# Performance work log

Hardware: AMD Instinct MI355X
Metric: run time of the kernel (lower is better)

Reference implementation:

```python
import jax, jax.numpy as jnp
import numpy as np

EPS = 1e-5  # torch LayerNorm default eps

def _mish(x):
    return x * jnp.tanh(jax.nn.softplus(x))

def _ln(x, g, b):
    mu = jnp.mean(x, axis=-1, keepdims=True)
    var = jnp.mean(jnp.square(x - mu), axis=-1, keepdims=True)
    return (x - mu) * jax.lax.rsqrt(var + EPS) * g + b

def setup_inputs() -> dict:
    key = jax.random.key(0)
    ks = jax.random.split(key, 10)
    B, D, O1, O2, O3 = 65536, 784, 512, 264, 128
    def lin(k, fan_in, shape):
        bound = 1.0 / np.sqrt(fan_in)
        return jax.random.uniform(k, shape, jnp.float32, -bound, bound)
    return {
        "x":  jax.random.uniform(ks[0], (B, D), jnp.float32),
        "W1": lin(ks[1], D,  (O1, D)),   # enFC1, bias=False
        "g1": jnp.ones((O1,), jnp.float32), "b1": jnp.zeros((O1,), jnp.float32),
        "W2": lin(ks[2], O1, (O2, O1)),  # enFC2, bias=False
        "g2": jnp.ones((O2,), jnp.float32), "b2": jnp.zeros((O2,), jnp.float32),
        "W3": lin(ks[3], O2, (O3, O2)),  # enFC3 with bias
        "b3": lin(ks[4], O2, (O3,)),
        "gh": jnp.ones((O3,), jnp.float32), "bh": jnp.zeros((O3,), jnp.float32),
        "D1": lin(ks[5], O3, (O2, O3)),  # deFC1, bias=False
        "g3": jnp.ones((O2,), jnp.float32), "b3n": jnp.zeros((O2,), jnp.float32),
        "D2": lin(ks[6], O2, (O1, O2)),  # deFC2, bias=False
        "g4": jnp.ones((O1,), jnp.float32), "b4": jnp.zeros((O1,), jnp.float32),
        "D3": lin(ks[7], O1, (D, O1)),   # deFC3 with bias
        "bo": lin(ks[8], O1, (D,)),
    }

def reference(x, W1, g1, b1, W2, g2, b2, W3, b3, gh, bh,
              D1, g3, b3n, D2, g4, b4, D3, bo):
    h = _mish(_ln(x @ W1.T, g1, b1))
    h = _mish(_ln(h @ W2.T, g2, b2))
    x_latent = _mish(_ln(h @ W3.T + b3, gh, bh))
    h = _mish(_ln(x_latent @ D1.T, g3, b3n))
    h = _mish(_ln(h @ D2.T, g4, b4))
    out = jax.nn.sigmoid(h @ D3.T + bo)
    return out, jnp.sum(jnp.abs(x_latent))
```

## Files before the change

### kernel.cpp

```cpp
#include <hip/hip_runtime.h>


typedef short bf16x8 __attribute__((ext_vector_type(8)));
typedef float f32x4  __attribute__((ext_vector_type(4)));

#define B_ROWS 65536
#define EPS_LN 1e-5f

static __device__ __forceinline__ unsigned short f2bf(float f) {
    union { float f; unsigned u; } v; v.f = f;
    unsigned r = v.u + 0x7FFFu + ((v.u >> 16) & 1u);
    return (unsigned short)(r >> 16);
}

static __device__ __forceinline__ float mish_f(float x) {
    if (x > 15.f) return x;
    float u = __expf(x);
    float p = __fmaf_rn(u, u, 2.f * u);
    return x * (p / (p + 2.f));
}

static __device__ __forceinline__ void glds16(const void* g, void* l) {
    typedef __attribute__((address_space(3))) unsigned lds_u32;
    typedef __attribute__((address_space(1))) const unsigned glb_u32;
    lds_u32* lp = (lds_u32*)l;
    unsigned lofs = __builtin_amdgcn_readfirstlane((unsigned)(unsigned long long)lp);
    lp = (lds_u32*)(unsigned long long)lofs;
    __builtin_amdgcn_global_load_lds((glb_u32*)g, lp, 16, 0, 0);
}

struct CvtArgs {
    const float* src[6];
    unsigned short* dst[6];
    int O[6], K[6], KP[6];
    int base[7];
};

__global__ void wpad_kernel(CvtArgs a) {
    int b = blockIdx.x;
    int seg = 0;
    while (b >= a.base[seg + 1]) ++seg;
    int r = b - a.base[seg];
    int O = a.O[seg], K = a.K[seg], KP = a.KP[seg];
    const float* s = a.src[seg];
    unsigned short* d = a.dst[seg];
    for (int c = threadIdx.x; c < KP; c += 256) {
        unsigned short v = 0;
        if (r < O && c < K) v = f2bf(s[(size_t)r * K + c]);
        d[(size_t)r * KP + c] = v;
    }
}

template<int KP, int ASTR, int KREAL, int OP, int OREAL, int OSTRIDE, int NKT,
         int NW, int WR, bool SRCF32, bool HASBIAS, bool ABS, bool LN>
__global__ __launch_bounds__(NW * 64, 4)
void layer5(const void* __restrict__ Asrc,
            const unsigned short* __restrict__ Wp,
            const float* __restrict__ gam,
            const float* __restrict__ bet,
            const float* __restrict__ bias,
            void* __restrict__ Aout,
            float* __restrict__ partials)
{
    constexpr int WC    = NW / WR;
    constexpr int NT    = OP / (WC * 16);
    constexpr int AR    = 4 / WR;
    constexpr int WROWS = 16 * AR;
    constexpr int NCH_W = OP / 16;
    constexpr int NCH   = NCH_W + (SRCF32 ? 0 : 4);
    constexpr int MAXC  = (NCH + NW - 1) / NW;
    constexpr int ABY   = 4096;
    constexpr int WBY   = OP * 64;

    __shared__ __align__(16) char smem[2 * ABY + 2 * WBY];

    const int tid  = threadIdx.x;
    const int wave = tid >> 6, lane = tid & 63;
    const int wrI = wave / WC, wcI = wave % WC;
    const int lg = lane >> 4, lc = lane & 15;
    const int row0  = blockIdx.x * 64;
    const int cbase = blockIdx.y * OP;

    const char* gp[MAXC];
#pragma unroll
    for (int i = 0; i < MAXC; ++i) {
        int c = wave + NW * i;
        gp[i] = nullptr;
        if (c < NCH_W) {
            int row = c * 16 + (lane >> 2);
            int sg = (lane & 3) ^ ((row >> 1) & 3);
            gp[i] = (const char*)Wp + ((size_t)(cbase + row) * KP + sg * 8) * 2;
        } else if (c < NCH) {
            int row = (c - NCH_W) * 16 + (lane >> 2);
            int sg = (lane & 3) ^ ((row >> 1) & 3);
            gp[i] = (const char*)Asrc + ((size_t)(row0 + row) * ASTR + sg * 8) * 2;
        }
    }
    auto stage = [&](int t, int b) {
#pragma unroll
        for (int i = 0; i < MAXC; ++i) {
            int c = wave + NW * i;
            if (c < NCH) {
                int off = (c < NCH_W) ? (2 * ABY + b * WBY + c * 1024)
                                      : (b * ABY + (c - NCH_W) * 1024);
                glds16(gp[i] + (size_t)t * 64, smem + off);
            }
        }
    };

    const int ar = tid >> 2, as = tid & 3;
    const float* axp = (const float*)Asrc + (size_t)(row0 + ar) * ASTR + as * 8;
    const int aswz = ar * 64 + ((as ^ ((ar >> 1) & 3)) << 4);
    float4 rA0 = make_float4(0,0,0,0), rA1 = make_float4(0,0,0,0);

    auto loadA1 = [&](int t) {
        int c0 = t * 32 + as * 8;
        rA0 = (c0     < KREAL) ? *(const float4*)(axp + t * 32)     : make_float4(0,0,0,0);
        rA1 = (c0 + 4 < KREAL) ? *(const float4*)(axp + t * 32 + 4) : make_float4(0,0,0,0);
    };
    auto pubA = [&](int b) {
        union { unsigned short us[8]; uint4 v; } u;
        u.us[0] = f2bf(rA0.x); u.us[1] = f2bf(rA0.y);
        u.us[2] = f2bf(rA0.z); u.us[3] = f2bf(rA0.w);
        u.us[4] = f2bf(rA1.x); u.us[5] = f2bf(rA1.y);
        u.us[6] = f2bf(rA1.z); u.us[7] = f2bf(rA1.w);
        *(uint4*)(smem + b * ABY + aswz) = u.v;
    };

    stage(0, 0);
    if constexpr (SRCF32) {
        if (tid < 256) { loadA1(0); pubA(0); if (NKT > 1) loadA1(1); }
    }
    __syncthreads();

    f32x4 acc[AR][NT];
#pragma unroll
    for (int a = 0; a < AR; ++a)
#pragma unroll
        for (int c = 0; c < NT; ++c) acc[a][c] = (f32x4){0.f, 0.f, 0.f, 0.f};

    const int fswz = ((lg ^ ((lc >> 1) & 3)) << 4);

    for (int t = 0; t < NKT; ++t) {
        const int bsel = t & 1;
        if (t + 1 < NKT) stage(t + 1, bsel ^ 1);

        const char* Ab = smem + bsel * ABY + (wrI * WROWS + lc) * 64 + fswz;
        const char* Bb = smem + 2 * ABY + bsel * WBY + (wcI * NT * 16 + lc) * 64 + fswz;
        bf16x8 afr[AR], bfr[NT];
#pragma unroll
        for (int a = 0; a < AR; ++a) afr[a] = *(const bf16x8*)(Ab + a * 1024);
#pragma unroll
        for (int c = 0; c < NT; ++c) bfr[c] = *(const bf16x8*)(Bb + c * 1024);

        if constexpr (SRCF32) {
            if (tid < 256) {
                if (t + 1 < NKT) pubA(bsel ^ 1);
                if (t + 2 < NKT) loadA1(t + 2);
            }
        }
#pragma unroll
        for (int c = 0; c < NT; ++c)
#pragma unroll
            for (int a = 0; a < AR; ++a)
                acc[a][c] = __builtin_amdgcn_mfma_f32_16x16x32_bf16(afr[a], bfr[c], acc[a][c], 0, 0, 0);
        __syncthreads();
    }

    if constexpr (LN) {
        if constexpr (HASBIAS) {
#pragma unroll
            for (int c = 0; c < NT; ++c) {
                int col = wcI * NT * 16 + c * 16 + lc;
                float bv = (col < OREAL) ? bias[col] : 0.f;
#pragma unroll
                for (int a = 0; a < AR; ++a)
#pragma unroll
                    for (int r = 0; r < 4; ++r) acc[a][c][r] += bv;
            }
        }
        float ps1[AR][4], ps2[AR][4];
#pragma unroll
        for (int a = 0; a < AR; ++a)
#pragma unroll
            for (int r = 0; r < 4; ++r) { ps1[a][r] = 0.f; ps2[a][r] = 0.f; }
#pragma unroll
        for (int a = 0; a < AR; ++a)
#pragma unroll
            for (int c = 0; c < NT; ++c)
#pragma unroll
                for (int r = 0; r < 4; ++r) {
                    float v = acc[a][c][r];
                    ps1[a][r] += v;
                    ps2[a][r] = __fmaf_rn(v, v, ps2[a][r]);
                }
#pragma unroll
        for (int m = 1; m < 16; m <<= 1)
#pragma unroll
            for (int a = 0; a < AR; ++a)
#pragma unroll
                for (int r = 0; r < 4; ++r) {
                    ps1[a][r] += __shfl_xor(ps1[a][r], m);
                    ps2[a][r] += __shfl_xor(ps2[a][r], m);
                }

        float* lnP   = (float*)smem;
        float* lnMR  = (float*)smem + 1024;
        float* wsumP = (float*)smem + 1152;

        if (lc == 0) {
#pragma unroll
            for (int a = 0; a < AR; ++a)
#pragma unroll
                for (int r = 0; r < 4; ++r) {
                    int row = a * 16 + lg * 4 + r;
                    lnP[row * 8 + wcI]       = ps1[a][r];
                    lnP[512 + row * 8 + wcI] = ps2[a][r];
                }
        }
        __syncthreads();
        if (tid < 64) {
            float s1 = 0.f, s2 = 0.f;
#pragma unroll
            for (int w = 0; w < WC; ++w) { s1 += lnP[tid * 8 + w]; s2 += lnP[512 + tid * 8 + w]; }
            float mu = s1 * (1.f / OREAL);
            float var = fmaxf(s2 * (1.f / OREAL) - mu * mu, 0.f);
            lnMR[tid]      = mu;
            lnMR[64 + tid] = rsqrtf(var + EPS_LN);
        }
        __syncthreads();

        float gcol[NT], bcol[NT];
#pragma unroll
        for (int c = 0; c < NT; ++c) {
            int col = wcI * NT * 16 + c * 16 + lc;
            gcol[c] = (col < OREAL) ? gam[col] : 0.f;
            bcol[c] = (col < OREAL) ? bet[col] : 0.f;
        }

        float asum = 0.f;
        unsigned short* outp = (unsigned short*)Aout;
#pragma unroll
        for (int a = 0; a < AR; ++a)
#pragma unroll
            for (int r = 0; r < 4; ++r) {
                int rl = a * 16 + lg * 4 + r;
                float mu = lnMR[rl], rs = lnMR[64 + rl];
                size_t rowoff = (size_t)(row0 + rl) * OSTRIDE;
#pragma unroll
                for (int c = 0; c < NT; ++c) {
                    int col = wcI * NT * 16 + c * 16 + lc;
                    if (col < OSTRIDE) {
                        unsigned short outv = 0;
                        if (col < OREAL) {
                            float v = (acc[a][c][r] - mu) * rs * gcol[c] + bcol[c];
                            float mz = mish_f(v);
                            if (ABS) asum += fabsf(mz);
                            outv = f2bf(mz);
                        }
                        outp[rowoff + col] = outv;
                    }
                }
            }

        if constexpr (ABS) {
#pragma unroll
            for (int m = 1; m < 64; m <<= 1) asum += __shfl_xor(asum, m);
            if (lane == 0) wsumP[wave] = asum;
            __syncthreads();
            if (tid == 0) {
                float s = 0.f;
                for (int w = 0; w < NW; ++w) s += wsumP[w];
                partials[blockIdx.x] = s;
            }
        }
    } else {
        float* outp = (float*)Aout;
#pragma unroll
        for (int c = 0; c < NT; ++c) {
            int col = cbase + wcI * NT * 16 + c * 16 + lc;
            bool ok = col < OREAL;
            float bv = ok ? bias[col] : 0.f;
#pragma unroll
            for (int a = 0; a < AR; ++a)
#pragma unroll
                for (int r = 0; r < 4; ++r) {
                    if (ok) {
                        int rl = wrI * WROWS + a * 16 + lg * 4 + r;
                        float v = acc[a][c][r] + bv;
                        outp[(size_t)(row0 + rl) * OSTRIDE + col] = 1.f / (1.f + __expf(-v));
                    }
                }
        }
    }
}

__global__ void reduce_abs(const float* __restrict__ partials, float* __restrict__ out) {
    __shared__ float sm[256];
    float s = 0.f;
    for (int i = threadIdx.x; i < 1024; i += 256) s += partials[i];
    sm[threadIdx.x] = s;
    __syncthreads();
    for (int step = 128; step > 0; step >>= 1) {
        if (threadIdx.x < step) sm[threadIdx.x] += sm[threadIdx.x + step];
        __syncthreads();
    }
    if (threadIdx.x == 0) out[0] = sm[0];
}

extern "C" void kernel_launch(void* const* d_in, const int* in_sizes, int n_in,
                              void* d_out, int out_size, void* d_ws, size_t ws_size,
                              hipStream_t stream)
{
    const float* x   = (const float*)d_in[0];
    const float* W1  = (const float*)d_in[1];
    const float* g1  = (const float*)d_in[2];
    const float* b1  = (const float*)d_in[3];
    const float* W2  = (const float*)d_in[4];
    const float* g2  = (const float*)d_in[5];
    const float* b2  = (const float*)d_in[6];
    const float* W3  = (const float*)d_in[7];
    const float* b3  = (const float*)d_in[8];
    const float* gh  = (const float*)d_in[9];
    const float* bh  = (const float*)d_in[10];
    const float* D1  = (const float*)d_in[11];
    const float* g3  = (const float*)d_in[12];
    const float* b3n = (const float*)d_in[13];
    const float* D2  = (const float*)d_in[14];
    const float* g4  = (const float*)d_in[15];
    const float* b4  = (const float*)d_in[16];
    const float* D3  = (const float*)d_in[17];
    const float* bo  = (const float*)d_in[18];

    char* ws = (char*)d_ws;
    size_t off = 0;
    auto alloc = [&](size_t bytes) -> char* {
        char* p = ws + off;
        off += (bytes + 255) & ~(size_t)255;
        return p;
    };
    unsigned short* W1p = (unsigned short*)alloc((size_t)512 * 800 * 2);
    unsigned short* W2p = (unsigned short*)alloc((size_t)384 * 512 * 2);
    unsigned short* W3p = (unsigned short*)alloc((size_t)128 * 288 * 2);
    unsigned short* D1p = (unsigned short*)alloc((size_t)384 * 128 * 2);
    unsigned short* D2p = (unsigned short*)alloc((size_t)512 * 288 * 2);
    unsigned short* D3p = (unsigned short*)alloc((size_t)896 * 512 * 2);
    unsigned short* actP = (unsigned short*)alloc((size_t)B_ROWS * 512 * 2);
    unsigned short* actQ = (unsigned short*)alloc((size_t)B_ROWS * 288 * 2);
    unsigned short* actL = (unsigned short*)alloc((size_t)B_ROWS * 128 * 2);
    float* partials = (float*)alloc(1024 * 4);

    CvtArgs ca;
    ca.src[0] = W1; ca.dst[0] = W1p; ca.O[0] = 512; ca.K[0] = 784; ca.KP[0] = 800;
    ca.src[1] = W2; ca.dst[1] = W2p; ca.O[1] = 264; ca.K[1] = 512; ca.KP[1] = 512;
    ca.src[2] = W3; ca.dst[2] = W3p; ca.O[2] = 128; ca.K[2] = 264; ca.KP[2] = 288;
    ca.src[3] = D1; ca.dst[3] = D1p; ca.O[3] = 264; ca.K[3] = 128; ca.KP[3] = 128;
    ca.src[4] = D2; ca.dst[4] = D2p; ca.O[4] = 512; ca.K[4] = 264; ca.KP[4] = 288;
    ca.src[5] = D3; ca.dst[5] = D3p; ca.O[5] = 784; ca.K[5] = 512; ca.KP[5] = 512;
    ca.base[0] = 0;    ca.base[1] = 512;  ca.base[2] = 896;
    ca.base[3] = 1024; ca.base[4] = 1408; ca.base[5] = 1920; ca.base[6] = 2816;
    wpad_kernel<<<2816, 256, 0, stream>>>(ca);

    const int NB = B_ROWS / 64;

    layer5<800, 784, 784, 512, 512, 512, 25, 8, 1, true,  false, false, true>
        <<<NB, 512, 0, stream>>>(x, W1p, g1, b1, nullptr, actP, nullptr);
    layer5<512, 512, 512, 384, 264, 288, 16, 8, 1, false, false, false, true>
        <<<NB, 512, 0, stream>>>(actP, W2p, g2, b2, nullptr, actQ, nullptr);
    layer5<288, 288, 288, 128, 128, 128, 9,  4, 1, false, true,  true,  true>
        <<<NB, 256, 0, stream>>>(actQ, W3p, gh, bh, b3, actL, partials);
    layer5<128, 128, 128, 384, 264, 288, 4,  8, 1, false, false, false, true>
        <<<NB, 512, 0, stream>>>(actL, D1p, g3, b3n, nullptr, actQ, nullptr);
    layer5<288, 288, 288, 512, 512, 512, 9,  8, 1, false, false, false, true>
        <<<NB, 512, 0, stream>>>(actQ, D2p, g4, b4, nullptr, actP, nullptr);
    dim3 g6(NB, 4);
    layer5<512, 512, 512, 224, 784, 784, 16, 4, 2, false, true,  false, false>
        <<<g6, 256, 0, stream>>>(actP, D3p, nullptr, nullptr, bo, d_out, nullptr);

    reduce_abs<<<1, 256, 0, stream>>>(partials, (float*)d_out + (size_t)B_ROWS * 784);
}
```

Measured before the change: 485.6 us.

## Use 16-wave blocks for all layers and pre-convert input to bf16

Adds a separate kernel that converts x to bf16 once, so the first layer can stage A through direct global-to-LDS loads instead of converting in-kernel from fp32. Every layer kernel now runs with 1024 threads (16 waves), which rearranges the wave-to-tile mapping and the LayerNorm partial reductions. The final layer is split into two launches over column ranges instead of a 4-wide grid. This trades an extra full pass over x (read fp32, write bf16) and larger blocks with higher register pressure for more in-flight waves and simpler staging.

```diff
diff --git a/kernel.cpp b/kernel.cpp
--- a/kernel.cpp
+++ b/kernel.cpp
@@ -27,6 +27,17 @@
     unsigned lofs = __builtin_amdgcn_readfirstlane((unsigned)(unsigned long long)lp);
     lp = (lds_u32*)(unsigned long long)lofs;
     __builtin_amdgcn_global_load_lds((glb_u32*)g, lp, 16, 0, 0);
+}
+
+__global__ __launch_bounds__(256)
+void cvtx_kernel(const float* __restrict__ x, unsigned short* __restrict__ xb) {
+    size_t i = ((size_t)blockIdx.x * 256 + threadIdx.x) * 8;
+    float4 a = *(const float4*)(x + i);
+    float4 b = *(const float4*)(x + i + 4);
+    union { unsigned short us[8]; uint4 v; } u;
+    u.us[0] = f2bf(a.x); u.us[1] = f2bf(a.y); u.us[2] = f2bf(a.z); u.us[3] = f2bf(a.w);
+    u.us[4] = f2bf(b.x); u.us[5] = f2bf(b.y); u.us[6] = f2bf(b.z); u.us[7] = f2bf(b.w);
+    *(uint4*)(xb + i) = u.v;
 }
 
 struct CvtArgs {
@@ -51,86 +62,60 @@
     }
 }
 
-template<int KP, int ASTR, int KREAL, int OP, int OREAL, int OSTRIDE, int NKT,
-         int NW, int WR, bool SRCF32, bool HASBIAS, bool ABS, bool LN>
-__global__ __launch_bounds__(NW * 64, 4)
-void layer5(const void* __restrict__ Asrc,
+template<int KP, int ASTR, int OP, int OREAL, int OSTRIDE, int NKT,
+         int WR, bool HASBIAS, bool ABS, bool LN>
+__global__ __launch_bounds__(1024, 8)
+void layer6(const unsigned short* __restrict__ Asrc,
             const unsigned short* __restrict__ Wp,
             const float* __restrict__ gam,
             const float* __restrict__ bet,
             const float* __restrict__ bias,
             void* __restrict__ Aout,
-            float* __restrict__ partials)
+            float* __restrict__ partials,
+            int cbase)
 {
-    constexpr int WC    = NW / WR;
+    constexpr int WC    = 16 / WR;
     constexpr int NT    = OP / (WC * 16);
     constexpr int AR    = 4 / WR;
     constexpr int WROWS = 16 * AR;
     constexpr int NCH_W = OP / 16;
-    constexpr int NCH   = NCH_W + (SRCF32 ? 0 : 4);
-    constexpr int MAXC  = (NCH + NW - 1) / NW;
+    constexpr int NCH   = NCH_W + 4;
+    constexpr int MAXC  = (NCH + 15) / 16;
     constexpr int ABY   = 4096;
     constexpr int WBY   = OP * 64;
 
     __shared__ __align__(16) char smem[2 * ABY + 2 * WBY];
 
     const int tid  = threadIdx.x;
-    const int wave = tid >> 6, lane = tid & 63;
-    const int wrI = wave / WC, wcI = wave % WC;
+    const int lane = tid & 63;
+    const int wu   = __builtin_amdgcn_readfirstlane(tid >> 6);
+    const int wrI = wu / WC, wcI = wu % WC;
     const int lg = lane >> 4, lc = lane & 15;
-    const int row0  = blockIdx.x * 64;
-    const int cbase = blockIdx.y * OP;
-
-    const char* gp[MAXC];
-#pragma unroll
-    for (int i = 0; i < MAXC; ++i) {
-        int c = wave + NW * i;
-        gp[i] = nullptr;
-        if (c < NCH_W) {
-            int row = c * 16 + (lane >> 2);
-            int sg = (lane & 3) ^ ((row >> 1) & 3);
-            gp[i] = (const char*)Wp + ((size_t)(cbase + row) * KP + sg * 8) * 2;
-        } else if (c < NCH) {
-            int row = (c - NCH_W) * 16 + (lane >> 2);
-            int sg = (lane & 3) ^ ((row >> 1) & 3);
-            gp[i] = (const char*)Asrc + ((size_t)(row0 + row) * ASTR + sg * 8) * 2;
-        }
-    }
+    const int row0 = blockIdx.x * 64;
+
+    const size_t vofW = (size_t)(((lane >> 2) * KP   + (((lane & 3) ^ ((lane >> 3) & 3)) << 3)) * 2);
+    const size_t vofA = (size_t)(((lane >> 2) * ASTR + (((lane & 3) ^ ((lane >> 3) & 3)) << 3)) * 2);
+
     auto stage = [&](int t, int b) {
 #pragma unroll
         for (int i = 0; i < MAXC; ++i) {
-            int c = wave + NW * i;
+            int c = wu + 16 * i;
             if (c < NCH) {
-                int off = (c < NCH_W) ? (2 * ABY + b * WBY + c * 1024)
-                                      : (b * ABY + (c - NCH_W) * 1024);
-                glds16(gp[i] + (size_t)t * 64, smem + off);
+                if (c < NCH_W) {
+                    const char* g = (const char*)Wp +
+                        ((size_t)(cbase + c * 16) * KP) * 2 + (size_t)t * 64 + vofW;
+                    glds16(g, smem + (2 * ABY + b * WBY + c * 1024));
+                } else {
+                    int ca = c - NCH_W;
+                    const char* g = (const char*)Asrc +
+                        ((size_t)(row0 + ca * 16) * ASTR) * 2 + (size_t)t * 64 + vofA;
+                    glds16(g, smem + (b * ABY + ca * 1024));
+                }
             }
         }
     };
 
-    const int ar = tid >> 2, as = tid & 3;
-    const float* axp = (const float*)Asrc + (size_t)(row0 + ar) * ASTR + as * 8;
-    const int aswz = ar * 64 + ((as ^ ((ar >> 1) & 3)) << 4);
-    float4 rA0 = make_float4(0,0,0,0), rA1 = make_float4(0,0,0,0);
-
-    auto loadA1 = [&](int t) {
-        int c0 = t * 32 + as * 8;
-        rA0 = (c0     < KREAL) ? *(const float4*)(axp + t * 32)     : make_float4(0,0,0,0);
-        rA1 = (c0 + 4 < KREAL) ? *(const float4*)(axp + t * 32 + 4) : make_float4(0,0,0,0);
-    };
-    auto pubA = [&](int b) {
-        union { unsigned short us[8]; uint4 v; } u;
-        u.us[0] = f2bf(rA0.x); u.us[1] = f2bf(rA0.y);
-        u.us[2] = f2bf(rA0.z); u.us[3] = f2bf(rA0.w);
-        u.us[4] = f2bf(rA1.x); u.us[5] = f2bf(rA1.y);
-        u.us[6] = f2bf(rA1.z); u.us[7] = f2bf(rA1.w);
-        *(uint4*)(smem + b * ABY + aswz) = u.v;
-    };
-
     stage(0, 0);
-    if constexpr (SRCF32) {
-        if (tid < 256) { loadA1(0); pubA(0); if (NKT > 1) loadA1(1); }
-    }
     __syncthreads();
 
     f32x4 acc[AR][NT];
@@ -153,12 +138,6 @@
 #pragma unroll
         for (int c = 0; c < NT; ++c) bfr[c] = *(const bf16x8*)(Bb + c * 1024);
 
-        if constexpr (SRCF32) {
-            if (tid < 256) {
-                if (t + 1 < NKT) pubA(bsel ^ 1);
-                if (t + 2 < NKT) loadA1(t + 2);
-            }
-        }
 #pragma unroll
         for (int c = 0; c < NT; ++c)
 #pragma unroll
@@ -205,24 +184,27 @@
                 }
 
         float* lnP   = (float*)smem;
-        float* lnMR  = (float*)smem + 1024;
-        float* wsumP = (float*)smem + 1152;
+        float* lnMR  = (float*)(smem + 8192);
+        float* wsumP = (float*)(smem + 8192 + 512);
 
         if (lc == 0) {
 #pragma unroll
             for (int a = 0; a < AR; ++a)
 #pragma unroll
                 for (int r = 0; r < 4; ++r) {
-                    int row = a * 16 + lg * 4 + r;
-                    lnP[row * 8 + wcI]       = ps1[a][r];
-                    lnP[512 + row * 8 + wcI] = ps2[a][r];
+                    int rl = wrI * WROWS + a * 16 + lg * 4 + r;
+                    lnP[rl * WC + wcI]           = ps1[a][r];
+                    lnP[64 * WC + rl * WC + wcI] = ps2[a][r];
                 }
         }
         __syncthreads();
         if (tid < 64) {
             float s1 = 0.f, s2 = 0.f;
 #pragma unroll
-            for (int w = 0; w < WC; ++w) { s1 += lnP[tid * 8 + w]; s2 += lnP[512 + tid * 8 + w]; }
+            for (int w = 0; w < WC; ++w) {
+                s1 += lnP[tid * WC + w];
+                s2 += lnP[64 * WC + tid * WC + w];
+            }
             float mu = s1 * (1.f / OREAL);
             float var = fmaxf(s2 * (1.f / OREAL) - mu * mu, 0.f);
             lnMR[tid]      = mu;
@@ -244,7 +226,7 @@
         for (int a = 0; a < AR; ++a)
 #pragma unroll
             for (int r = 0; r < 4; ++r) {
-                int rl = a * 16 + lg * 4 + r;
+                int rl = wrI * WROWS + a * 16 + lg * 4 + r;
                 float mu = lnMR[rl], rs = lnMR[64 + rl];
                 size_t rowoff = (size_t)(row0 + rl) * OSTRIDE;
 #pragma unroll
@@ -266,11 +248,11 @@
         if constexpr (ABS) {
 #pragma unroll
             for (int m = 1; m < 64; m <<= 1) asum += __shfl_xor(asum, m);
-            if (lane == 0) wsumP[wave] = asum;
+            if (lane == 0) wsumP[tid >> 6] = asum;
             __syncthreads();
             if (tid == 0) {
                 float s = 0.f;
-                for (int w = 0; w < NW; ++w) s += wsumP[w];
+                for (int w = 0; w < 16; ++w) s += wsumP[w];
                 partials[blockIdx.x] = s;
             }
         }
@@ -345,10 +327,13 @@
     unsigned short* D1p = (unsigned short*)alloc((size_t)384 * 128 * 2);
     unsigned short* D2p = (unsigned short*)alloc((size_t)512 * 288 * 2);
     unsigned short* D3p = (unsigned short*)alloc((size_t)896 * 512 * 2);
-    unsigned short* actP = (unsigned short*)alloc((size_t)B_ROWS * 512 * 2);
-    unsigned short* actQ = (unsigned short*)alloc((size_t)B_ROWS * 288 * 2);
-    unsigned short* actL = (unsigned short*)alloc((size_t)B_ROWS * 128 * 2);
+    unsigned short* xbf = (unsigned short*)alloc((size_t)B_ROWS * 784 * 2 + 256);
+    unsigned short* actP = (unsigned short*)alloc((size_t)B_ROWS * 512 * 2 + 256);
+    unsigned short* actQ = (unsigned short*)alloc((size_t)B_ROWS * 288 * 2 + 256);
+    unsigned short* actL = (unsigned short*)alloc((size_t)B_ROWS * 128 * 2 + 256);
     float* partials = (float*)alloc(1024 * 4);
+
+    cvtx_kernel<<<25088, 256, 0, stream>>>(x, xbf);
 
     CvtArgs ca;
     ca.src[0] = W1; ca.dst[0] = W1p; ca.O[0] = 512; ca.K[0] = 784; ca.KP[0] = 800;
@@ -363,19 +348,20 @@
 
     const int NB = B_ROWS / 64;
 
-    layer5<800, 784, 784, 512, 512, 512, 25, 8, 1, true,  false, false, true>
-        <<<NB, 512, 0, stream>>>(x, W1p, g1, b1, nullptr, actP, nullptr);
-    layer5<512, 512, 512, 384, 264, 288, 16, 8, 1, false, false, false, true>
-        <<<NB, 512, 0, stream>>>(actP, W2p, g2, b2, nullptr, actQ, nullptr);
-    layer5<288, 288, 288, 128, 128, 128, 9,  4, 1, false, true,  true,  true>
-        <<<NB, 256, 0, stream>>>(actQ, W3p, gh, bh, b3, actL, partials);
-    layer5<128, 128, 128, 384, 264, 288, 4,  8, 1, false, false, false, true>
-        <<<NB, 512, 0, stream>>>(actL, D1p, g3, b3n, nullptr, actQ, nullptr);
-    layer5<288, 288, 288, 512, 512, 512, 9,  8, 1, false, false, false, true>
-        <<<NB, 512, 0, stream>>>(actQ, D2p, g4, b4, nullptr, actP, nullptr);
-    dim3 g6(NB, 4);
-    layer5<512, 512, 512, 224, 784, 784, 16, 4, 2, false, true,  false, false>
-        <<<g6, 256, 0, stream>>>(actP, D3p, nullptr, nullptr, bo, d_out, nullptr);
+    layer6<800, 784, 512, 512, 512, 25, 1, false, false, true>
+        <<<NB, 1024, 0, stream>>>(xbf, W1p, g1, b1, nullptr, actP, nullptr, 0);
+    layer6<512, 512, 384, 264, 288, 16, 2, false, false, true>
+        <<<NB, 1024, 0, stream>>>(actP, W2p, g2, b2, nullptr, actQ, nullptr, 0);
+    layer6<288, 288, 128, 128, 128, 9, 2, true, true, true>
+        <<<NB, 1024, 0, stream>>>(actQ, W3p, gh, bh, b3, actL, partials, 0);
+    layer6<128, 128, 384, 264, 288, 4, 2, false, false, true>
+        <<<NB, 1024, 0, stream>>>(actL, D1p, g3, b3n, nullptr, actQ, nullptr, 0);
+    layer6<288, 288, 512, 512, 512, 9, 1, false, false, true>
+        <<<NB, 1024, 0, stream>>>(actQ, D2p, g4, b4, nullptr, actP, nullptr, 0);
+    layer6<512, 512, 512, 784, 784, 16, 1, true, false, false>
+        <<<NB, 1024, 0, stream>>>(actP, D3p, nullptr, nullptr, bo, d_out, nullptr, 0);
+    layer6<512, 512, 384, 784, 784, 16, 2, true, false, false>
+        <<<NB, 1024, 0, stream>>>(actP, D3p, nullptr, nullptr, bo, d_out, nullptr, 512);
 
     reduce_abs<<<1, 256, 0, stream>>>(partials, (float*)d_out + (size_t)B_ROWS * 784);
 }
```

Result: slower. 636.5 us (+31.1%).

## Fuse all six MLP layers into one persistent-per-tile megakernel with LDS activations

Applied to the files above, without the earlier changes.

Replaces six separate layer launches with a single 1024-thread kernel per 64-row tile. The tile's intermediate activations stay in LDS (about 148 KB) and are never written to or reread from global memory. This targets the HBM traffic for the bf16 intermediates and the per-launch overhead. The cost is one block per CU with a large LDS footprint, lower occupancy, and weights restaged from global/L2 for every tile, so latency hiding depends on the in-block double buffering.

```diff
diff --git a/kernel.cpp b/kernel.cpp
--- a/kernel.cpp
+++ b/kernel.cpp
@@ -51,72 +51,87 @@
     }
 }
 
-template<int KP, int ASTR, int KREAL, int OP, int OREAL, int OSTRIDE, int NKT,
-         int NW, int WR, bool SRCF32, bool HASBIAS, bool ABS, bool LN>
-__global__ __launch_bounds__(NW * 64, 4)
-void layer5(const void* __restrict__ Asrc,
-            const unsigned short* __restrict__ Wp,
-            const float* __restrict__ gam,
-            const float* __restrict__ bet,
-            const float* __restrict__ bias,
-            void* __restrict__ Aout,
-            float* __restrict__ partials)
-{
-    constexpr int WC    = NW / WR;
-    constexpr int NT    = OP / (WC * 16);
-    constexpr int AR    = 4 / WR;
-    constexpr int WROWS = 16 * AR;
-    constexpr int NCH_W = OP / 16;
-    constexpr int NCH   = NCH_W + (SRCF32 ? 0 : 4);
-    constexpr int MAXC  = (NCH + NW - 1) / NW;
-    constexpr int ABY   = 4096;
-    constexpr int WBY   = OP * 64;
-
-    __shared__ __align__(16) char smem[2 * ABY + 2 * WBY];
-
-    const int tid  = threadIdx.x;
-    const int wave = tid >> 6, lane = tid & 63;
-    const int wrI = wave / WC, wcI = wave % WC;
-    const int lg = lane >> 4, lc = lane & 15;
-    const int row0  = blockIdx.x * 64;
-    const int cbase = blockIdx.y * OP;
-
-    const char* gp[MAXC];
-#pragma unroll
-    for (int i = 0; i < MAXC; ++i) {
-        int c = wave + NW * i;
-        gp[i] = nullptr;
-        if (c < NCH_W) {
-            int row = c * 16 + (lane >> 2);
-            int sg = (lane & 3) ^ ((row >> 1) & 3);
-            gp[i] = (const char*)Wp + ((size_t)(cbase + row) * KP + sg * 8) * 2;
-        } else if (c < NCH) {
-            int row = (c - NCH_W) * 16 + (lane >> 2);
-            int sg = (lane & 3) ^ ((row >> 1) & 3);
-            gp[i] = (const char*)Asrc + ((size_t)(row0 + row) * ASTR + sg * 8) * 2;
-        }
-    }
+template<int NKT, int OP, int KP, int WSTB, bool WDB, int ABASE, int ASTRLDS>
+__device__ __forceinline__ void gemm_h(char* smem,
+    const unsigned short* __restrict__ Wp, int cbase,
+    int lane, int wu, int wrI, int wcI, int lg, int lc, int fswz,
+    f32x4 (&acc)[2][OP / 128])
+{
+    constexpr int NT = OP / 128, NCHW = OP / 16, MAXC = (NCHW + 15) / 16;
+    constexpr int WBY = OP * 64;
+    const size_t vofW = ((size_t)(lane >> 2) * KP +
+                         (size_t)((((lane & 3) ^ ((lane >> 3) & 3))) << 3)) * 2;
     auto stage = [&](int t, int b) {
 #pragma unroll
         for (int i = 0; i < MAXC; ++i) {
-            int c = wave + NW * i;
-            if (c < NCH) {
-                int off = (c < NCH_W) ? (2 * ABY + b * WBY + c * 1024)
-                                      : (b * ABY + (c - NCH_W) * 1024);
-                glds16(gp[i] + (size_t)t * 64, smem + off);
+            int c = wu + 16 * i;
+            if (c < NCHW) {
+                const char* g = (const char*)Wp +
+                    ((size_t)(cbase + c * 16) * KP) * 2 + (size_t)t * 64 + vofW;
+                glds16(g, smem + WSTB + (WDB ? b * WBY : 0) + c * 1024);
             }
         }
     };
-
+    if constexpr (WDB) stage(0, 0);
+    __syncthreads();
+    for (int t = 0; t < NKT; ++t) {
+        int bsel = 0;
+        if constexpr (WDB) {
+            bsel = t & 1;
+            if (t + 1 < NKT) stage(t + 1, bsel ^ 1);
+        } else {
+            stage(t, 0);
+            __syncthreads();
+        }
+        bf16x8 afr[2], bfr[NT];
+#pragma unroll
+        for (int a = 0; a < 2; ++a) {
+            int arow = wrI * 32 + a * 16 + lc;
+            afr[a] = *(const bf16x8*)(smem + ABASE + arow * ASTRLDS + t * 64 + fswz);
+        }
+#pragma unroll
+        for (int c = 0; c < NT; ++c) {
+            int wrow = wcI * (NT * 16) + c * 16 + lc;
+            bfr[c] = *(const bf16x8*)(smem + WSTB + (WDB ? bsel * WBY : 0) + wrow * 64 + fswz);
+        }
+#pragma unroll
+        for (int c = 0; c < NT; ++c)
+#pragma unroll
+            for (int a = 0; a < 2; ++a)
+                acc[a][c] = __builtin_amdgcn_mfma_f32_16x16x32_bf16(afr[a], bfr[c], acc[a][c], 0, 0, 0);
+        __syncthreads();
+    }
+}
+
+template<int NKT, int OP, int KP, int WSTB, int ABASE>
+__device__ __forceinline__ void gemm_f32(char* smem,
+    const unsigned short* __restrict__ Wp, const float* __restrict__ x, int row0,
+    int tid, int lane, int wu, int wrI, int wcI, int lg, int lc, int fswz,
+    f32x4 (&acc)[2][OP / 128])
+{
+    constexpr int NT = OP / 128, NCHW = OP / 16, MAXC = (NCHW + 15) / 16;
+    constexpr int WBY = OP * 64;
+    const size_t vofW = ((size_t)(lane >> 2) * KP +
+                         (size_t)((((lane & 3) ^ ((lane >> 3) & 3))) << 3)) * 2;
+    auto stage = [&](int t, int b) {
+#pragma unroll
+        for (int i = 0; i < MAXC; ++i) {
+            int c = wu + 16 * i;
+            if (c < NCHW) {
+                const char* g = (const char*)Wp +
+                    ((size_t)c * 16 * KP) * 2 + (size_t)t * 64 + vofW;
+                glds16(g, smem + WSTB + b * WBY + c * 1024);
+            }
+        }
+    };
     const int ar = tid >> 2, as = tid & 3;
-    const float* axp = (const float*)Asrc + (size_t)(row0 + ar) * ASTR + as * 8;
+    const float* axp = x + (size_t)(row0 + ar) * 784 + as * 8;
     const int aswz = ar * 64 + ((as ^ ((ar >> 1) & 3)) << 4);
-    float4 rA0 = make_float4(0,0,0,0), rA1 = make_float4(0,0,0,0);
-
+    float4 rA0 = make_float4(0, 0, 0, 0), rA1 = make_float4(0, 0, 0, 0);
     auto loadA1 = [&](int t) {
         int c0 = t * 32 + as * 8;
-        rA0 = (c0     < KREAL) ? *(const float4*)(axp + t * 32)     : make_float4(0,0,0,0);
-        rA1 = (c0 + 4 < KREAL) ? *(const float4*)(axp + t * 32 + 4) : make_float4(0,0,0,0);
+        rA0 = (c0     < 784) ? *(const float4*)(axp + t * 32)     : make_float4(0, 0, 0, 0);
+        rA1 = (c0 + 4 < 784) ? *(const float4*)(axp + t * 32 + 4) : make_float4(0, 0, 0, 0);
     };
     auto pubA = [&](int b) {
         union { unsigned short us[8]; uint4 v; } u;
@@ -124,174 +139,269 @@
         u.us[2] = f2bf(rA0.z); u.us[3] = f2bf(rA0.w);
         u.us[4] = f2bf(rA1.x); u.us[5] = f2bf(rA1.y);
         u.us[6] = f2bf(rA1.z); u.us[7] = f2bf(rA1.w);
-        *(uint4*)(smem + b * ABY + aswz) = u.v;
+        *(uint4*)(smem + ABASE + b * 4096 + aswz) = u.v;
     };
-
     stage(0, 0);
-    if constexpr (SRCF32) {
-        if (tid < 256) { loadA1(0); pubA(0); if (NKT > 1) loadA1(1); }
-    }
-    __syncthreads();
-
-    f32x4 acc[AR][NT];
-#pragma unroll
-    for (int a = 0; a < AR; ++a)
-#pragma unroll
-        for (int c = 0; c < NT; ++c) acc[a][c] = (f32x4){0.f, 0.f, 0.f, 0.f};
-
-    const int fswz = ((lg ^ ((lc >> 1) & 3)) << 4);
-
+    if (tid < 256) { loadA1(0); pubA(0); if (NKT > 1) loadA1(1); }
+    __syncthreads();
     for (int t = 0; t < NKT; ++t) {
         const int bsel = t & 1;
         if (t + 1 < NKT) stage(t + 1, bsel ^ 1);
-
-        const char* Ab = smem + bsel * ABY + (wrI * WROWS + lc) * 64 + fswz;
-        const char* Bb = smem + 2 * ABY + bsel * WBY + (wcI * NT * 16 + lc) * 64 + fswz;
-        bf16x8 afr[AR], bfr[NT];
-#pragma unroll
-        for (int a = 0; a < AR; ++a) afr[a] = *(const bf16x8*)(Ab + a * 1024);
-#pragma unroll
-        for (int c = 0; c < NT; ++c) bfr[c] = *(const bf16x8*)(Bb + c * 1024);
-
-        if constexpr (SRCF32) {
-            if (tid < 256) {
-                if (t + 1 < NKT) pubA(bsel ^ 1);
-                if (t + 2 < NKT) loadA1(t + 2);
-            }
+        bf16x8 afr[2], bfr[NT];
+#pragma unroll
+        for (int a = 0; a < 2; ++a) {
+            int arow = wrI * 32 + a * 16 + lc;
+            afr[a] = *(const bf16x8*)(smem + ABASE + bsel * 4096 + arow * 64 + fswz);
+        }
+#pragma unroll
+        for (int c = 0; c < NT; ++c) {
+            int wrow = wcI * (NT * 16) + c * 16 + lc;
+            bfr[c] = *(const bf16x8*)(smem + WSTB + bsel * WBY + wrow * 64 + fswz);
+        }
+        if (tid < 256) {
+            if (t + 1 < NKT) pubA(bsel ^ 1);
+            if (t + 2 < NKT) loadA1(t + 2);
         }
 #pragma unroll
         for (int c = 0; c < NT; ++c)
 #pragma unroll
-            for (int a = 0; a < AR; ++a)
+            for (int a = 0; a < 2; ++a)
                 acc[a][c] = __builtin_amdgcn_mfma_f32_16x16x32_bf16(afr[a], bfr[c], acc[a][c], 0, 0, 0);
         __syncthreads();
     }
-
-    if constexpr (LN) {
-        if constexpr (HASBIAS) {
+}
+
+template<int OP, int OREAL, int OSTR, int HBASE, int HSTR, int SCR, bool HB, bool ABS>
+__device__ __forceinline__ void ln_epi(char* smem, f32x4 (&acc)[2][OP / 128],
+    const float* __restrict__ gam, const float* __restrict__ bet,
+    const float* __restrict__ bias, float* __restrict__ partials,
+    int tid, int lane, int wu, int wrI, int wcI, int lg, int lc, int bidx)
+{
+    constexpr int NT = OP / 128;
+    if constexpr (HB) {
+#pragma unroll
+        for (int c = 0; c < NT; ++c) {
+            int col = wcI * (NT * 16) + c * 16 + lc;
+            float bv = (col < OREAL) ? bias[col] : 0.f;
+#pragma unroll
+            for (int a = 0; a < 2; ++a)
+#pragma unroll
+                for (int r = 0; r < 4; ++r) acc[a][c][r] += bv;
+        }
+    }
+    float ps1[2][4], ps2[2][4];
+#pragma unroll
+    for (int a = 0; a < 2; ++a)
+#pragma unroll
+        for (int r = 0; r < 4; ++r) { ps1[a][r] = 0.f; ps2[a][r] = 0.f; }
+#pragma unroll
+    for (int a = 0; a < 2; ++a)
+#pragma unroll
+        for (int c = 0; c < NT; ++c)
+#pragma unroll
+            for (int r = 0; r < 4; ++r) {
+                float v = acc[a][c][r];
+                ps1[a][r] += v;
+                ps2[a][r] = __fmaf_rn(v, v, ps2[a][r]);
+            }
+#pragma unroll
+    for (int m = 1; m < 16; m <<= 1)
+#pragma unroll
+        for (int a = 0; a < 2; ++a)
+#pragma unroll
+            for (int r = 0; r < 4; ++r) {
+                ps1[a][r] += __shfl_xor(ps1[a][r], m);
+                ps2[a][r] += __shfl_xor(ps2[a][r], m);
+            }
+    float* lnP  = (float*)(smem + SCR);
+    float* lnMR = (float*)(smem + SCR + 4096);
+    float* wsum = (float*)(smem + SCR + 4608);
+    if (lc == 0) {
+#pragma unroll
+        for (int a = 0; a < 2; ++a)
+#pragma unroll
+            for (int r = 0; r < 4; ++r) {
+                int row = wrI * 32 + a * 16 + lg * 4 + r;
+                lnP[row * 8 + wcI]       = ps1[a][r];
+                lnP[512 + row * 8 + wcI] = ps2[a][r];
+            }
+    }
+    __syncthreads();
+    if (tid < 64) {
+        float s1 = 0.f, s2 = 0.f;
+#pragma unroll
+        for (int w = 0; w < 8; ++w) { s1 += lnP[tid * 8 + w]; s2 += lnP[512 + tid * 8 + w]; }
+        float mu = s1 * (1.f / OREAL);
+        float var = fmaxf(s2 * (1.f / OREAL) - mu * mu, 0.f);
+        lnMR[tid]      = mu;
+        lnMR[64 + tid] = rsqrtf(var + EPS_LN);
+    }
+    __syncthreads();
+    float gcol[NT], bcol[NT];
+#pragma unroll
+    for (int c = 0; c < NT; ++c) {
+        int col = wcI * (NT * 16) + c * 16 + lc;
+        gcol[c] = (col < OREAL) ? gam[col] : 0.f;
+        bcol[c] = (col < OREAL) ? bet[col] : 0.f;
+    }
+    float asum = 0.f;
+#pragma unroll
+    for (int a = 0; a < 2; ++a)
+#pragma unroll
+        for (int r = 0; r < 4; ++r) {
+            int rowl = wrI * 32 + a * 16 + lg * 4 + r;
+            float mu = lnMR[rowl], rs = lnMR[64 + rowl];
+            int sx = (rowl >> 1) & 3;
+            int rowb = HBASE + rowl * HSTR;
 #pragma unroll
             for (int c = 0; c < NT; ++c) {
-                int col = wcI * NT * 16 + c * 16 + lc;
-                float bv = (col < OREAL) ? bias[col] : 0.f;
-#pragma unroll
-                for (int a = 0; a < AR; ++a)
-#pragma unroll
-                    for (int r = 0; r < 4; ++r) acc[a][c][r] += bv;
-            }
-        }
-        float ps1[AR][4], ps2[AR][4];
-#pragma unroll
-        for (int a = 0; a < AR; ++a)
-#pragma unroll
-            for (int r = 0; r < 4; ++r) { ps1[a][r] = 0.f; ps2[a][r] = 0.f; }
-#pragma unroll
-        for (int a = 0; a < AR; ++a)
-#pragma unroll
-            for (int c = 0; c < NT; ++c)
-#pragma unroll
-                for (int r = 0; r < 4; ++r) {
-                    float v = acc[a][c][r];
-                    ps1[a][r] += v;
-                    ps2[a][r] = __fmaf_rn(v, v, ps2[a][r]);
+                int col = wcI * (NT * 16) + c * 16 + lc;
+                if (col < OSTR) {
+                    unsigned short outv = 0;
+                    if (col < OREAL) {
+                        float v = (acc[a][c][r] - mu) * rs * gcol[c] + bcol[c];
+                        float mz = mish_f(v);
+                        if (ABS) asum += fabsf(mz);
+                        outv = f2bf(mz);
+                    }
+                    int byte = rowb + ((col >> 5) << 6) +
+                               ((((col >> 3) & 3) ^ sx) << 4) + ((col & 7) << 1);
+                    *(unsigned short*)(smem + byte) = outv;
                 }
-#pragma unroll
-        for (int m = 1; m < 16; m <<= 1)
-#pragma unroll
-            for (int a = 0; a < AR; ++a)
-#pragma unroll
-                for (int r = 0; r < 4; ++r) {
-                    ps1[a][r] += __shfl_xor(ps1[a][r], m);
-                    ps2[a][r] += __shfl_xor(ps2[a][r], m);
+            }
+        }
+    if constexpr (ABS) {
+#pragma unroll
+        for (int m = 1; m < 64; m <<= 1) asum += __shfl_xor(asum, m);
+        if (lane == 0) wsum[wu] = asum;
+        __syncthreads();
+        if (tid == 0) {
+            float s = 0.f;
+            for (int w = 0; w < 16; ++w) s += wsum[w];
+            partials[bidx] = s;
+        }
+    }
+    __syncthreads();
+}
+
+template<int OP, int CB>
+__device__ __forceinline__ void out_epi(f32x4 (&acc)[2][OP / 128],
+    const float* __restrict__ bo, float* __restrict__ outp, int row0,
+    int wrI, int wcI, int lg, int lc)
+{
+    constexpr int NT = OP / 128;
+#pragma unroll
+    for (int c = 0; c < NT; ++c) {
+        int col = CB + wcI * (NT * 16) + c * 16 + lc;
+        bool ok = col < 784;
+        float bv = ok ? bo[col] : 0.f;
+#pragma unroll
+        for (int a = 0; a < 2; ++a)
+#pragma unroll
+            for (int r = 0; r < 4; ++r) {
+                if (ok) {
+                    int rowl = wrI * 32 + a * 16 + lg * 4 + r;
+                    float v = acc[a][c][r] + bv;
+                    outp[(size_t)(row0 + rowl) * 784 + col] = 1.f / (1.f + __expf(-v));
                 }
-
-        float* lnP   = (float*)smem;
-        float* lnMR  = (float*)smem + 1024;
-        float* wsumP = (float*)smem + 1152;
-
-        if (lc == 0) {
-#pragma unroll
-            for (int a = 0; a < AR; ++a)
-#pragma unroll
-                for (int r = 0; r < 4; ++r) {
-                    int row = a * 16 + lg * 4 + r;
-                    lnP[row * 8 + wcI]       = ps1[a][r];
-                    lnP[512 + row * 8 + wcI] = ps2[a][r];
-                }
-        }
-        __syncthreads();
-        if (tid < 64) {
-            float s1 = 0.f, s2 = 0.f;
-#pragma unroll
-            for (int w = 0; w < WC; ++w) { s1 += lnP[tid * 8 + w]; s2 += lnP[512 + tid * 8 + w]; }
-            float mu = s1 * (1.f / OREAL);
-            float var = fmaxf(s2 * (1.f / OREAL) - mu * mu, 0.f);
-            lnMR[tid]      = mu;
-            lnMR[64 + tid] = rsqrtf(var + EPS_LN);
-        }
-        __syncthreads();
-
-        float gcol[NT], bcol[NT];
-#pragma unroll
-        for (int c = 0; c < NT; ++c) {
-            int col = wcI * NT * 16 + c * 16 + lc;
-            gcol[c] = (col < OREAL) ? gam[col] : 0.f;
-            bcol[c] = (col < OREAL) ? bet[col] : 0.f;
-        }
-
-        float asum = 0.f;
-        unsigned short* outp = (unsigned short*)Aout;
-#pragma unroll
-        for (int a = 0; a < AR; ++a)
-#pragma unroll
-            for (int r = 0; r < 4; ++r) {
-                int rl = a * 16 + lg * 4 + r;
-                float mu = lnMR[rl], rs = lnMR[64 + rl];
-                size_t rowoff = (size_t)(row0 + rl) * OSTRIDE;
-#pragma unroll
-                for (int c = 0; c < NT; ++c) {
-                    int col = wcI * NT * 16 + c * 16 + lc;
-                    if (col < OSTRIDE) {
-                        unsigned short outv = 0;
-                        if (col < OREAL) {
-                            float v = (acc[a][c][r] - mu) * rs * gcol[c] + bcol[c];
-                            float mz = mish_f(v);
-                            if (ABS) asum += fabsf(mz);
-                            outv = f2bf(mz);
-                        }
-                        outp[rowoff + col] = outv;
-                    }
-                }
-            }
-
-        if constexpr (ABS) {
-#pragma unroll
-            for (int m = 1; m < 64; m <<= 1) asum += __shfl_xor(asum, m);
-            if (lane == 0) wsumP[wave] = asum;
-            __syncthreads();
-            if (tid == 0) {
-                float s = 0.f;
-                for (int w = 0; w < NW; ++w) s += wsumP[w];
-                partials[blockIdx.x] = s;
-            }
-        }
-    } else {
-        float* outp = (float*)Aout;
-#pragma unroll
-        for (int c = 0; c < NT; ++c) {
-            int col = cbase + wcI * NT * 16 + c * 16 + lc;
-            bool ok = col < OREAL;
-            float bv = ok ? bias[col] : 0.f;
-#pragma unroll
-            for (int a = 0; a < AR; ++a)
-#pragma unroll
-                for (int r = 0; r < 4; ++r) {
-                    if (ok) {
-                        int rl = wrI * WROWS + a * 16 + lg * 4 + r;
-                        float v = acc[a][c][r] + bv;
-                        outp[(size_t)(row0 + rl) * OSTRIDE + col] = 1.f / (1.f + __expf(-v));
-                    }
-                }
-        }
+            }
+    }
+    __syncthreads();
+}
+
+struct NetArgs {
+    const float* x;
+    const unsigned short *W1, *W2, *W3, *D1, *D2, *D3;
+    const float *g1, *b1, *g2, *b2, *gh, *bh, *b3, *g3, *b3n, *g4, *b4, *bo;
+    float* out;
+    float* partials;
+};
+
+__global__ __launch_bounds__(1024)
+void meganet(NetArgs A)
+{
+    __shared__ __align__(16) char smem[151552];
+    const int tid  = threadIdx.x;
+    const int lane = tid & 63;
+    const int wu   = __builtin_amdgcn_readfirstlane(tid >> 6);
+    const int wrI = wu >> 3, wcI = wu & 7;
+    const int lg = lane >> 4, lc = lane & 15;
+    const int fswz = ((lg ^ ((lc >> 1) & 3)) << 4);
+    const int row0 = blockIdx.x * 64;
+    const int bidx = blockIdx.x;
+
+    {
+        f32x4 acc[2][4];
+#pragma unroll
+        for (int a = 0; a < 2; ++a)
+#pragma unroll
+            for (int c = 0; c < 4; ++c) acc[a][c] = (f32x4){0.f, 0.f, 0.f, 0.f};
+        gemm_f32<25, 512, 800, 73728, 65536>(smem, A.W1, A.x, row0,
+            tid, lane, wu, wrI, wcI, lg, lc, fswz, acc);
+        ln_epi<512, 512, 512, 0, 1024, 73728, false, false>(smem, acc,
+            A.g1, A.b1, nullptr, nullptr, tid, lane, wu, wrI, wcI, lg, lc, bidx);
+    }
+    {
+        f32x4 acc[2][3];
+#pragma unroll
+        for (int a = 0; a < 2; ++a)
+#pragma unroll
+            for (int c = 0; c < 3; ++c) acc[a][c] = (f32x4){0.f, 0.f, 0.f, 0.f};
+        gemm_h<16, 384, 512, 102400, true, 0, 1024>(smem, A.W2, 0,
+            lane, wu, wrI, wcI, lg, lc, fswz, acc);
+        ln_epi<384, 264, 288, 65536, 576, 102400, false, false>(smem, acc,
+            A.g2, A.b2, nullptr, nullptr, tid, lane, wu, wrI, wcI, lg, lc, bidx);
+    }
+    {
+        f32x4 acc[2][1];
+#pragma unroll
+        for (int a = 0; a < 2; ++a) acc[a][0] = (f32x4){0.f, 0.f, 0.f, 0.f};
+        gemm_h<9, 128, 288, 102400, true, 65536, 576>(smem, A.W3, 0,
+            lane, wu, wrI, wcI, lg, lc, fswz, acc);
+        ln_epi<128, 128, 128, 0, 256, 102400, true, true>(smem, acc,
+            A.gh, A.bh, A.b3, A.partials, tid, lane, wu, wrI, wcI, lg, lc, bidx);
+    }
+    {
+        f32x4 acc[2][3];
+#pragma unroll
+        for (int a = 0; a < 2; ++a)
+#pragma unroll
+            for (int c = 0; c < 3; ++c) acc[a][c] = (f32x4){0.f, 0.f, 0.f, 0.f};
+        gemm_h<4, 384, 128, 16384, true, 0, 256>(smem, A.D1, 0,
+            lane, wu, wrI, wcI, lg, lc, fswz, acc);
+        ln_epi<384, 264, 288, 65536, 576, 16384, false, false>(smem, acc,
+            A.g3, A.b3n, nullptr, nullptr, tid, lane, wu, wrI, wcI, lg, lc, bidx);
+    }
+    {
+        f32x4 acc[2][4];
+#pragma unroll
+        for (int a = 0; a < 2; ++a)
+#pragma unroll
+            for (int c = 0; c < 4; ++c) acc[a][c] = (f32x4){0.f, 0.f, 0.f, 0.f};
+        gemm_h<9, 512, 288, 102400, false, 65536, 576>(smem, A.D2, 0,
+            lane, wu, wrI, wcI, lg, lc, fswz, acc);
+        ln_epi<512, 512, 512, 0, 1024, 102400, false, false>(smem, acc,
+            A.g4, A.b4, nullptr, nullptr, tid, lane, wu, wrI, wcI, lg, lc, bidx);
+    }
+    {
+        f32x4 acc[2][4];
+#pragma unroll
+        for (int a = 0; a < 2; ++a)
+#pragma unroll
+            for (int c = 0; c < 4; ++c) acc[a][c] = (f32x4){0.f, 0.f, 0.f, 0.f};
+        gemm_h<16, 512, 512, 65536, true, 0, 1024>(smem, A.D3, 0,
+            lane, wu, wrI, wcI, lg, lc, fswz, acc);
+        out_epi<512, 0>(acc, A.bo, A.out, row0, wrI, wcI, lg, lc);
+    }
+    {
+        f32x4 acc[2][3];
+#pragma unroll
+        for (int a = 0; a < 2; ++a)
+#pragma unroll
+            for (int c = 0; c < 3; ++c) acc[a][c] = (f32x4){0.f, 0.f, 0.f, 0.f};
+        gemm_h<16, 384, 512, 65536, true, 0, 1024>(smem, A.D3, 512,
+            lane, wu, wrI, wcI, lg, lc, fswz, acc);
+        out_epi<384, 512>(acc, A.bo, A.out, row0, wrI, wcI, lg, lc);
     }
 }
 
@@ -345,9 +455,6 @@
     unsigned short* D1p = (unsigned short*)alloc((size_t)384 * 128 * 2);
     unsigned short* D2p = (unsigned short*)alloc((size_t)512 * 288 * 2);
     unsigned short* D3p = (unsigned short*)alloc((size_t)896 * 512 * 2);
-    unsigned short* actP = (unsigned short*)alloc((size_t)B_ROWS * 512 * 2);
-    unsigned short* actQ = (unsigned short*)alloc((size_t)B_ROWS * 288 * 2);
-    unsigned short* actL = (unsigned short*)alloc((size_t)B_ROWS * 128 * 2);
     float* partials = (float*)alloc(1024 * 4);
 
     CvtArgs ca;
@@ -361,21 +468,16 @@
     ca.base[3] = 1024; ca.base[4] = 1408; ca.base[5] = 1920; ca.base[6] = 2816;
     wpad_kernel<<<2816, 256, 0, stream>>>(ca);
 
-    const int NB = B_ROWS / 64;
-
-    layer5<800, 784, 784, 512, 512, 512, 25, 8, 1, true,  false, false, true>
-        <<<NB, 512, 0, stream>>>(x, W1p, g1, b1, nullptr, actP, nullptr);
-    layer5<512, 512, 512, 384, 264, 288, 16, 8, 1, false, false, false, true>
-        <<<NB, 512, 0, stream>>>(actP, W2p, g2, b2, nullptr, actQ, nullptr);
-    layer5<288, 288, 288, 128, 128, 128, 9,  4, 1, false, true,  true,  true>
-        <<<NB, 256, 0, stream>>>(actQ, W3p, gh, bh, b3, actL, partials);
-    layer5<128, 128, 128, 384, 264, 288, 4,  8, 1, false, false, false, true>
-        <<<NB, 512, 0, stream>>>(actL, D1p, g3, b3n, nullptr, actQ, nullptr);
-    layer5<288, 288, 288, 512, 512, 512, 9,  8, 1, false, false, false, true>
-        <<<NB, 512, 0, stream>>>(actQ, D2p, g4, b4, nullptr, actP, nullptr);
-    dim3 g6(NB, 4);
-    layer5<512, 512, 512, 224, 784, 784, 16, 4, 2, false, true,  false, false>
-        <<<g6, 256, 0, stream>>>(actP, D3p, nullptr, nullptr, bo, d_out, nullptr);
+    NetArgs na;
+    na.x = x;
+    na.W1 = W1p; na.W2 = W2p; na.W3 = W3p; na.D1 = D1p; na.D2 = D2p; na.D3 = D3p;
+    na.g1 = g1; na.b1 = b1; na.g2 = g2; na.b2 = b2;
+    na.gh = gh; na.bh = bh; na.b3 = b3;
+    na.g3 = g3; na.b3n = b3n; na.g4 = g4; na.b4 = b4; na.bo = bo;
+    na.out = (float*)d_out;
+    na.partials = partials;
+
+    meganet<<<B_ROWS / 64, 1024, 0, stream>>>(na);
 
     reduce_abs<<<1, 256, 0, stream>>>(partials, (float*)d_out + (size_t)B_ROWS * 784);
 }
```

Result: slower. 540.1 us (+11.2%).
